# Kernel optimization log

Measured on AMD Instinct MI355X. Metric: run time of the kernel, lower is better.

## Reference

```python
import jax, jax.numpy as jnp
import numpy as np

N = 20000      # nodes per graph
E = 320000     # edges per graph (before self-loops)
G = 256        # graphs (strings) per side
VOCAB = 128    # NUMBER_EMBEDDINGS
D_IN = 128
HID = 64
H = 4
D_OUT = 128
NEG_SLOPE = 0.2  # PyG GATConv leaky_relu slope


def _gat(x, edge_index, W, att_s, att_d, bias, concat):
    """PyG GATConv: gather -> per-edge logits -> segment softmax over dst -> scatter.
    x: [N, F_in], W: [F_in, H*C], att_s/att_d: [H, C], bias: [H*C] or [C].
    Self-loops are added (PyG default add_self_loops=True)."""
    n = x.shape[0]
    h, c = att_s.shape
    loops = jnp.arange(n)
    src = jnp.concatenate([edge_index[0], loops])  # message sources j
    dst = jnp.concatenate([edge_index[1], loops])  # message targets i
    xh = (x @ W).reshape(n, h, c)                  # [N,H,C]
    a_s = jnp.einsum('nhc,hc->nh', xh, att_s)      # [N,H]
    a_d = jnp.einsum('nhc,hc->nh', xh, att_d)
    logits = jax.nn.leaky_relu(a_s[src] + a_d[dst], NEG_SLOPE)  # [E',H]
    m = jax.ops.segment_max(logits, dst, num_segments=n)
    m = jnp.where(jnp.isfinite(m), m, 0.0)
    e = jnp.exp(logits - m[dst])
    z = jax.ops.segment_sum(e, dst, num_segments=n)
    alpha = e / (z[dst] + 1e-16)                   # [E',H]
    msg = xh[src] * alpha[:, :, None]              # [E',H,C]
    out = jax.ops.segment_sum(msg, dst, num_segments=n)  # [N,H,C]
    out = out.reshape(n, h * c) if concat else out.mean(axis=1)
    return out + bias


def _encode(xi, ei, batch, emb, W1, as1, ad1, b1, lw1, lb1,
            W2, as2, ad2, b2, lw2, lb2, W3, as3, ad3, b3, lw3, lb3):
    e = emb[xi]  # [N, D_IN]
    x = jax.nn.relu(_gat(e, ei, W1, as1, ad1, b1, True) + e @ lw1 + lb1)
    x = jax.nn.relu(_gat(x, ei, W2, as2, ad2, b2, True) + x @ lw2 + lb2)
    x = _gat(x, ei, W3, as3, ad3, b3, False) + x @ lw3 + lb3  # [N, D_OUT]
    s = jax.ops.segment_sum(x, batch, num_segments=G)
    cnt = jax.ops.segment_sum(jnp.ones((x.shape[0],), x.dtype), batch, num_segments=G)
    return s / jnp.maximum(cnt, 1.0)[:, None]  # global_mean_pool -> [G, D_OUT]


def setup_inputs() -> dict:
    key = jax.random.key(0)
    ks = jax.random.split(key, 32)
    hc = H * HID  # 256
    def nrm(k, shape, scale=0.05):
        return jax.random.normal(k, shape, dtype=jnp.float32) * scale
    inp = {
        'x_l': jax.random.randint(ks[0], (N,), 0, VOCAB),
        'edge_l': jax.random.randint(ks[1], (2, E), 0, N),
        'batch_l': jnp.sort(jax.random.randint(ks[2], (N,), 0, G)),
        'x_r': jax.random.randint(ks[3], (N,), 0, VOCAB),
        'edge_r': jax.random.randint(ks[4], (2, E), 0, N),
        'batch_r': jnp.sort(jax.random.randint(ks[5], (N,), 0, G)),
        'emb': nrm(ks[6], (VOCAB, D_IN), 1.0),
        'W1': nrm(ks[7], (D_IN, hc)), 'as1': nrm(ks[8], (H, HID)), 'ad1': nrm(ks[9], (H, HID)),
        'b1': jnp.zeros((hc,), jnp.float32), 'lw1': nrm(ks[10], (D_IN, hc)), 'lb1': jnp.zeros((hc,), jnp.float32),
        'W2': nrm(ks[11], (hc, hc)), 'as2': nrm(ks[12], (H, HID)), 'ad2': nrm(ks[13], (H, HID)),
        'b2': jnp.zeros((hc,), jnp.float32), 'lw2': nrm(ks[14], (hc, hc)), 'lb2': jnp.zeros((hc,), jnp.float32),
        'W3': nrm(ks[15], (hc, H * D_OUT)), 'as3': nrm(ks[16], (H, D_OUT)), 'ad3': nrm(ks[17], (H, D_OUT)),
        'b3': jnp.zeros((D_OUT,), jnp.float32), 'lw3': nrm(ks[18], (hc, D_OUT)), 'lb3': jnp.zeros((D_OUT,), jnp.float32),
    }
    return inp


def reference(x_l, edge_l, batch_l, x_r, edge_r, batch_r, emb,
              W1, as1, ad1, b1, lw1, lb1,
              W2, as2, ad2, b2, lw2, lb2,
              W3, as3, ad3, b3, lw3, lb3):
    params = (emb, W1, as1, ad1, b1, lw1, lb1, W2, as2, ad2, b2, lw2, lb2,
              W3, as3, ad3, b3, lw3, lb3)
    out_l = _encode(x_l, edge_l, batch_l, *params)
    out_r = _encode(x_r, edge_r, batch_r, *params)
    return (out_l, out_r)
```

## Files before the change

kernel.cpp:

```cpp
#include <hip/hip_runtime.h>

#define GG 256

typedef __bf16 bf16x8 __attribute__((ext_vector_type(8)));
typedef float floatx4 __attribute__((ext_vector_type(4)));
typedef float f32x2 __attribute__((ext_vector_type(2)));

__device__ __forceinline__ float lrelu(float x) { return x > 0.f ? x : 0.2f * x; }

__device__ __forceinline__ void wt1(const float* __restrict__ B, __bf16* __restrict__ Bt,
                                    int K, int M, int idx) {
    int k = idx / M, m = idx - k * M;
    Bt[(size_t)m * K + k] = (__bf16)B[idx];
}
__device__ __forceinline__ void wattn1(const float* __restrict__ W,
                                       const float* __restrict__ as_,
                                       const float* __restrict__ ad_,
                                       __bf16* __restrict__ dst, int K, int C, int idx) {
    int j = idx / K, k = idx - j * K;
    float v = 0.f;
    if (j < 8) {
        int h = j & 3;
        const float* att = (j < 4) ? as_ : ad_;
        int M = 4 * C;
        for (int c = 0; c < C; c++) v += W[(size_t)k * M + h * C + c] * att[h * C + c];
    }
    dst[(size_t)j * K + k] = (__bf16)v;
}

__global__ void k_wprep(const float* W1, const float* lw1, const float* as1, const float* ad1,
                        const float* W2, const float* lw2, const float* as2, const float* ad2,
                        const float* W3, const float* lw3, const float* as3, const float* ad3,
                        __bf16* B1t, __bf16* B2t, __bf16* B3t) {
    int idx = blockIdx.x * blockDim.x + threadIdx.x;
    if (idx < 32768) { wt1(W1, B1t, 128, 256, idx); return; }
    idx -= 32768;
    if (idx < 32768) { wt1(lw1, B1t + 256 * 128, 128, 256, idx); return; }
    idx -= 32768;
    if (idx < 2048) { wattn1(W1, as1, ad1, B1t + 512 * 128, 128, 64, idx); return; }
    idx -= 2048;
    if (idx < 65536) { wt1(W2, B2t, 256, 256, idx); return; }
    idx -= 65536;
    if (idx < 65536) { wt1(lw2, B2t + 256 * 256, 256, 256, idx); return; }
    idx -= 65536;
    if (idx < 4096) { wattn1(W2, as2, ad2, B2t + 512 * 256, 256, 64, idx); return; }
    idx -= 4096;
    if (idx < 131072) { wt1(W3, B3t, 256, 512, idx); return; }
    idx -= 131072;
    if (idx < 32768) { wt1(lw3, B3t + 512 * 256, 256, 128, idx); return; }
    idx -= 32768;
    if (idx < 4096) { wattn1(W3, as3, ad3, B3t + 640 * 256, 256, 128, idx); return; }
}

template <int K, bool EMB>
__global__ __launch_bounds__(256) void k_gemm_all(const __bf16* __restrict__ A,
                                                  const int* __restrict__ xl,
                                                  const int* __restrict__ xr,
                                                  const float* __restrict__ emb,
                                                  const __bf16* __restrict__ Bt,
                                                  int n, int n1, int Mx, int Ml,
                                                  unsigned char* __restrict__ x8, int ldx,
                                                  float* __restrict__ lin, int ldl,
                                                  const float* __restrict__ bias1,
                                                  const float* __restrict__ bias2,
                                                  float* __restrict__ a_s,
                                                  float* __restrict__ a_d) {
    constexpr int KS = K / 32;
    constexpr int LDK = K + 8;
    constexpr int LPR = K / 8;
    constexpr int NCH = 64 * LPR / 256;
    __shared__ __bf16 S[64 * LDK];
    int tid = threadIdx.x;
    int wave = tid >> 6, lane = tid & 63;
    int row0 = blockIdx.x * 64;
#pragma unroll
    for (int c = 0; c < NCH; c++) {
        int i = tid + c * 256;
        int r = i / LPR, ko = (i - r * LPR) * 8;
        int gr = row0 + r;
        bf16x8 v = {};
        if (gr < n) {
            if (EMB) {
                int xi = (gr < n1) ? xl[gr] : xr[gr - n1];
                const float4* src = (const float4*)(emb + ((size_t)xi << 7) + ko);
                float4 q0 = src[0], q1 = src[1];
                v = bf16x8{(__bf16)q0.x, (__bf16)q0.y, (__bf16)q0.z, (__bf16)q0.w,
                           (__bf16)q1.x, (__bf16)q1.y, (__bf16)q1.z, (__bf16)q1.w};
            } else {
                v = *(const bf16x8*)(A + (size_t)gr * K + ko);
            }
        }
        *(bf16x8*)&S[r * LDK + ko] = v;
    }
    __syncthreads();
    int kOff = (lane >> 4) * 8;
    int colBase = lane & 15;
    bf16x8 af[KS];
#pragma unroll
    for (int ks = 0; ks < KS; ks++)
        af[ks] = *(const bf16x8*)&S[(wave * 16 + colBase) * LDK + ks * 32 + kOff];
    int Mtot = Mx + Ml;
    int gr0 = row0 + wave * 16 + ((lane >> 4) << 2);
    int half = (Mtot / 128) * 64;
    int c0beg = blockIdx.y * half;
    int T = half / 64;
    bf16x8 regs[NCH];
#pragma unroll
    for (int c = 0; c < NCH; c++) {
        int i = tid + c * 256;
        int r = i / LPR, ko = (i - r * LPR) * 8;
        regs[c] = *(const bf16x8*)(Bt + (size_t)(c0beg + r) * K + ko);
    }
    for (int t = 0; t < T; t++) {
        __syncthreads();
#pragma unroll
        for (int c = 0; c < NCH; c++) {
            int i = tid + c * 256;
            int r = i / LPR, ko = (i - r * LPR) * 8;
            *(bf16x8*)&S[r * LDK + ko] = regs[c];
        }
        if (t + 1 < T) {
            int c0n = c0beg + (t + 1) * 64;
#pragma unroll
            for (int c = 0; c < NCH; c++) {
                int i = tid + c * 256;
                int r = i / LPR, ko = (i - r * LPR) * 8;
                regs[c] = *(const bf16x8*)(Bt + (size_t)(c0n + r) * K + ko);
            }
        }
        __syncthreads();
        floatx4 acc[4] = {};
#pragma unroll
        for (int ct = 0; ct < 4; ct++) {
#pragma unroll
            for (int ks = 0; ks < KS; ks++) {
                bf16x8 bf = *(const bf16x8*)&S[(ct * 16 + colBase) * LDK + ks * 32 + kOff];
                acc[ct] = __builtin_amdgcn_mfma_f32_16x16x32_bf16(af[ks], bf, acc[ct], 0, 0, 0);
            }
        }
        int c0 = c0beg + t * 64;
        if (c0 < Mx) {
#pragma unroll
            for (int r = 0; r < 4; r++) {
                int gr = gr0 + r;
                if (gr >= n) continue;
#pragma unroll
                for (int ct = 0; ct < 4; ct++) {
                    float v = acc[ct][r];
                    int p = __builtin_amdgcn_cvt_pk_fp8_f32(v, v, 0, false);
                    x8[(size_t)gr * ldx + c0 + ct * 16 + colBase] = (unsigned char)(p & 0xff);
                }
            }
        } else {
#pragma unroll
            for (int r = 0; r < 4; r++) {
                int gr = gr0 + r;
                if (gr >= n) continue;
#pragma unroll
                for (int ct = 0; ct < 4; ct++) {
                    int c2 = c0 + ct * 16 + colBase - Mx;
                    float v = acc[ct][r] + bias1[c2];
                    if (bias2) v += bias2[c2];
                    lin[(size_t)gr * ldl + c2] = v;
                }
            }
        }
    }
    if (blockIdx.y == 1) {
        floatx4 acc = {};
        const __bf16* bp = Bt + (size_t)(Mtot + colBase) * K + kOff;
#pragma unroll
        for (int ks = 0; ks < KS; ks++) {
            bf16x8 bf = *(const bf16x8*)(bp + ks * 32);
            acc = __builtin_amdgcn_mfma_f32_16x16x32_bf16(af[ks], bf, acc, 0, 0, 0);
        }
        if (colBase < 8) {
            float* dst = (colBase < 4) ? a_s : a_d;
            int h = colBase & 3;
#pragma unroll
            for (int r = 0; r < 4; r++) {
                int gr = gr0 + r;
                if (gr < n) dst[gr * 4 + h] = acc[r];
            }
        }
    }
}

__global__ void k_hist2(const int* __restrict__ el, const int* __restrict__ er,
                        int E, int n, int* __restrict__ deg) {
    int e = blockIdx.x * blockDim.x + threadIdx.x;
    if (e >= 2 * E) return;
    int d = (e < E) ? el[E + e] : er[E + (e - E)] + n;
    atomicAdd(&deg[d], 1);
}

__global__ __launch_bounds__(1024) void k_scan(int* __restrict__ rp, int n) {
    __shared__ int wsum[16];
    __shared__ int s_carry;
    int lane = threadIdx.x & 63, wid = threadIdx.x >> 6;
    if (threadIdx.x == 0) s_carry = 0;
    __syncthreads();
    for (int base = 0; base < n; base += 1024) {
        int i = base + threadIdx.x;
        int v = (i < n) ? rp[i] : 0;
        int inc = v;
#pragma unroll
        for (int off = 1; off < 64; off <<= 1) {
            int t = __shfl_up(inc, off, 64);
            if (lane >= off) inc += t;
        }
        if (lane == 63) wsum[wid] = inc;
        __syncthreads();
        int carry = s_carry;
        __syncthreads();
        if (wid == 0) {
            int wv = (lane < 16) ? wsum[lane] : 0;
            int winc = wv;
#pragma unroll
            for (int off = 1; off < 16; off <<= 1) {
                int t = __shfl_up(winc, off, 64);
                if (lane >= off) winc += t;
            }
            if (lane < 16) wsum[lane] = winc - wv;
            if (lane == 15) s_carry = carry + winc;
        }
        __syncthreads();
        if (i < n) rp[i] = carry + wsum[wid] + (inc - v);
        __syncthreads();
    }
}

__global__ void k_fill2(const int* __restrict__ el, const int* __restrict__ er,
                        int E, int n, int* __restrict__ rp, int* __restrict__ csr) {
    int e = blockIdx.x * blockDim.x + threadIdx.x;
    if (e >= 2 * E) return;
    int d, s;
    if (e < E) { s = el[e]; d = el[E + e]; }
    else       { s = er[e - E] + n; d = er[E + (e - E)] + n; }
    int pos = atomicAdd(&rp[d], 1);
    csr[pos] = s;
}

__device__ __forceinline__ void dec4(unsigned int u, float* f) {
    f32x2 a = __builtin_amdgcn_cvt_pk_f32_fp8(u, false);
    f32x2 b = __builtin_amdgcn_cvt_pk_f32_fp8(u, true);
    f[0] = a[0]; f[1] = a[1]; f[2] = b[0]; f[3] = b[1];
}

__global__ __launch_bounds__(256) void k_agg12(const int* __restrict__ rp,
                                               const int* __restrict__ csr,
                                               const float* __restrict__ a_s,
                                               const float* __restrict__ a_d,
                                               const unsigned char* __restrict__ x8,
                                               const float* __restrict__ lin,
                                               __bf16* __restrict__ out_bf, int n) {
    int wv = (int)((blockIdx.x * blockDim.x + threadIdx.x) >> 6);
    int lane = threadIdx.x & 63;
    int sub = lane >> 5, sl = lane & 31;
    int node = wv * 2 + sub;
    if (node >= n) return;
    int c0 = sl * 8;
    int h = sl >> 3;
    int start = node ? rp[node - 1] : 0;
    int end = rp[node];
    float ad = a_d[node * 4 + h];
    float z = __expf(lrelu(a_s[node * 4 + h] + ad));
    float acc[8];
    {
        uint2 u = *(const uint2*)(x8 + (size_t)node * 256 + c0);
        float f[8];
        dec4(u.x, f); dec4(u.y, f + 4);
#pragma unroll
        for (int j = 0; j < 8; j++) acc[j] = z * f[j];
    }
    uint2 u0 = {}, u1 = {};
    float A0 = 0.f, A1 = 0.f;
    if (start < end) {
        int s = csr[start];
        u0 = *(const uint2*)(x8 + (size_t)s * 256 + c0);
        A0 = a_s[s * 4 + h];
    }
    if (start + 1 < end) {
        int s = csr[start + 1];
        u1 = *(const uint2*)(x8 + (size_t)s * 256 + c0);
        A1 = a_s[s * 4 + h];
    }
    for (int e = start; e < end; e++) {
        uint2 uc = u0;
        float ac = A0;
        u0 = u1; A0 = A1;
        if (e + 2 < end) {
            int s = csr[e + 2];
            u1 = *(const uint2*)(x8 + (size_t)s * 256 + c0);
            A1 = a_s[s * 4 + h];
        }
        float w = __expf(lrelu(ac + ad));
        z += w;
        float f[8];
        dec4(uc.x, f); dec4(uc.y, f + 4);
#pragma unroll
        for (int q = 0; q < 8; q++) acc[q] += w * f[q];
    }
    float inv = 1.f / (z + 1e-16f);
    const float4* lp = (const float4*)(lin + (size_t)node * 256 + c0);
    float4 l0 = lp[0], l1 = lp[1];
    float lf[8] = {l0.x, l0.y, l0.z, l0.w, l1.x, l1.y, l1.z, l1.w};
    bf16x8 r;
#pragma unroll
    for (int j = 0; j < 8; j++)
        r[j] = (__bf16)fmaxf(acc[j] * inv + lf[j], 0.f);
    *(bf16x8*)(out_bf + (size_t)node * 256 + c0) = r;
}

__global__ __launch_bounds__(256) void k_agg3(const int* __restrict__ rp,
                                              const int* __restrict__ csr,
                                              const float* __restrict__ a_s,
                                              const float* __restrict__ a_d,
                                              const unsigned int* __restrict__ x8,
                                              float* __restrict__ mean, int n) {
    int wv = (int)((blockIdx.x * blockDim.x + threadIdx.x) >> 6);
    int lane = threadIdx.x & 63;
    int sub = lane >> 5, sl = lane & 31;
    int node = wv * 2 + sub;
    if (node >= n) return;
    int h = sl >> 3;
    int start = node ? rp[node - 1] : 0;
    int end = rp[node];
    float ad = a_d[node * 4 + h];
    float z = __expf(lrelu(a_s[node * 4 + h] + ad));
    float acc[16];
    {
        uint4 u = *(const uint4*)(x8 + (size_t)node * 128 + sl * 4);
        float f[16];
        dec4(u.x, f); dec4(u.y, f + 4); dec4(u.z, f + 8); dec4(u.w, f + 12);
#pragma unroll
        for (int j = 0; j < 16; j++) acc[j] = z * f[j];
    }
    uint4 u0 = {}, u1 = {};
    float A0 = 0.f, A1 = 0.f;
    if (start < end) {
        int s = csr[start];
        u0 = *(const uint4*)(x8 + (size_t)s * 128 + sl * 4);
        A0 = a_s[s * 4 + h];
    }
    if (start + 1 < end) {
        int s = csr[start + 1];
        u1 = *(const uint4*)(x8 + (size_t)s * 128 + sl * 4);
        A1 = a_s[s * 4 + h];
    }
    for (int e = start; e < end; e++) {
        uint4 uc = u0;
        float ac = A0;
        u0 = u1; A0 = A1;
        if (e + 2 < end) {
            int s = csr[e + 2];
            u1 = *(const uint4*)(x8 + (size_t)s * 128 + sl * 4);
            A1 = a_s[s * 4 + h];
        }
        float w = __expf(lrelu(ac + ad));
        z += w;
        float f[16];
        dec4(uc.x, f); dec4(uc.y, f + 4); dec4(uc.z, f + 8); dec4(uc.w, f + 12);
#pragma unroll
        for (int q = 0; q < 16; q++) acc[q] += w * f[q];
    }
    float scale = 0.25f / (z + 1e-16f);
#pragma unroll
    for (int j = 0; j < 16; j++) {
        float v = acc[j] * scale;
        v += __shfl_xor(v, 8, 64);
        v += __shfl_xor(v, 16, 64);
        acc[j] = v;
    }
    if ((sl & 24) == 0) {
        float4* op = (float4*)(mean + (size_t)node * 128 + sl * 16);
#pragma unroll
        for (int q = 0; q < 4; q++) {
            float4 o = {acc[4 * q], acc[4 * q + 1], acc[4 * q + 2], acc[4 * q + 3]};
            op[q] = o;
        }
    }
}

__global__ __launch_bounds__(128) void k_pool(const float* __restrict__ mean,
                                              const float* __restrict__ lin3,
                                              const float* __restrict__ b3,
                                              const int* __restrict__ bl,
                                              const int* __restrict__ br,
                                              int n, float* __restrict__ out) {
    int g = blockIdx.x, c = threadIdx.x;
    const int* b = (g < GG) ? bl : br;
    int tg = (g < GG) ? g : g - GG;
    int off = (g < GG) ? 0 : n;
    int s, e;
    { int lo = 0, hi = n; while (lo < hi) { int m = (lo + hi) >> 1; if (b[m] < tg) lo = m + 1; else hi = m; } s = lo; }
    { int lo = 0, hi = n; while (lo < hi) { int m = (lo + hi) >> 1; if (b[m] < tg + 1) lo = m + 1; else hi = m; } e = lo; }
    s += off; e += off;
    float acc = 0.f;
    for (int i = s; i < e; i++)
        acc += mean[(size_t)i * 128 + c] + lin3[(size_t)i * 128 + c];
    int cnt = e - s;
    out[(size_t)g * 128 + c] = cnt > 0 ? acc / (float)cnt + b3[c] : 0.f;
}

static inline int cdiv(int a, int b) { return (a + b - 1) / b; }

extern "C" void kernel_launch(void* const* d_in, const int* in_sizes, int n_in,
                              void* d_out, int out_size, void* d_ws, size_t ws_size,
                              hipStream_t stream) {
    const int* x_l = (const int*)d_in[0];
    const int* edge_l = (const int*)d_in[1];
    const int* batch_l = (const int*)d_in[2];
    const int* x_r = (const int*)d_in[3];
    const int* edge_r = (const int*)d_in[4];
    const int* batch_r = (const int*)d_in[5];
    const float* emb = (const float*)d_in[6];
    const float* W1 = (const float*)d_in[7];
    const float* as1 = (const float*)d_in[8];
    const float* ad1 = (const float*)d_in[9];
    const float* b1 = (const float*)d_in[10];
    const float* lw1 = (const float*)d_in[11];
    const float* lb1 = (const float*)d_in[12];
    const float* W2 = (const float*)d_in[13];
    const float* as2 = (const float*)d_in[14];
    const float* ad2 = (const float*)d_in[15];
    const float* b2 = (const float*)d_in[16];
    const float* lw2 = (const float*)d_in[17];
    const float* lb2 = (const float*)d_in[18];
    const float* W3 = (const float*)d_in[19];
    const float* as3 = (const float*)d_in[20];
    const float* ad3 = (const float*)d_in[21];
    const float* b3 = (const float*)d_in[22];
    const float* lw3 = (const float*)d_in[23];
    const float* lb3 = (const float*)d_in[24];

    const int n = in_sizes[0];
    const int E = in_sizes[1] / 2;
    const int N2 = 2 * n;

    float* MEAN = (float*)d_ws;
    float* LIN = MEAN + (size_t)N2 * 128;
    float* L3 = LIN + (size_t)N2 * 256;
    float* a_s = L3 + (size_t)N2 * 128;
    float* a_d = a_s + (size_t)N2 * 4;
    int* rp = (int*)(a_d + (size_t)N2 * 4);
    int* csr = rp + N2;
    unsigned char* X8a = (unsigned char*)(csr + 2 * E);
    unsigned char* X8b = X8a + (size_t)N2 * 256;
    __bf16* Abf = (__bf16*)(X8b + (size_t)N2 * 512);
    __bf16* B1t = Abf + (size_t)N2 * 256;
    __bf16* B2t = B1t + 528 * 128;
    __bf16* B3t = B2t + 528 * 256;

    const int TB = 256;
    dim3 blk(TB);

    k_wprep<<<cdiv(370688, TB), blk, 0, stream>>>(W1, lw1, as1, ad1, W2, lw2, as2, ad2,
                                                  W3, lw3, as3, ad3, B1t, B2t, B3t);

    hipMemsetAsync(rp, 0, sizeof(int) * (size_t)N2, stream);
    k_hist2<<<cdiv(2 * E, TB), blk, 0, stream>>>(edge_l, edge_r, E, n, rp);
    k_scan<<<1, 1024, 0, stream>>>(rp, N2);
    k_fill2<<<cdiv(2 * E, TB), blk, 0, stream>>>(edge_l, edge_r, E, n, rp, csr);

    k_gemm_all<128, true><<<dim3(cdiv(N2, 64), 2), blk, 0, stream>>>(
        nullptr, x_l, x_r, emb, B1t, N2, n, 256, 256, X8a, 256, LIN, 256, lb1, b1, a_s, a_d);
    k_agg12<<<cdiv(N2, 8), blk, 0, stream>>>(rp, csr, a_s, a_d, X8a, LIN, Abf, N2);

    k_gemm_all<256, false><<<dim3(cdiv(N2, 64), 2), blk, 0, stream>>>(
        Abf, nullptr, nullptr, nullptr, B2t, N2, n, 256, 256, X8a, 256, LIN, 256, lb2, b2, a_s, a_d);
    k_agg12<<<cdiv(N2, 8), blk, 0, stream>>>(rp, csr, a_s, a_d, X8a, LIN, Abf, N2);

    k_gemm_all<256, false><<<dim3(cdiv(N2, 64), 2), blk, 0, stream>>>(
        Abf, nullptr, nullptr, nullptr, B3t, N2, n, 512, 128, X8b, 512, L3, 128, lb3, nullptr, a_s, a_d);
    k_agg3<<<cdiv(N2, 8), blk, 0, stream>>>(rp, csr, a_s, a_d, (const unsigned int*)X8b, MEAN, N2);
    k_pool<<<2 * GG, 128, 0, stream>>>(MEAN, L3, b3, batch_l, batch_r, n, (float*)d_out);
}
```

Before: 498.8 us.

## Enlarge GEMM row tile, store linear branch in bf16, one node per wave

Each GEMM block now covers 128 rows instead of 64, with two MFMA row tiles per wave sharing each B fragment, which halves B-tile reloads per output. The layer 1 and 2 linear/residual outputs are stored as bf16 rather than fp32, cutting write and read traffic. The aggregation kernels now give each node a full 64-lane wave instead of half a wave, with a deeper 3-edge prefetch pipeline. The trade-offs are more registers and LDS per GEMM block, fewer GEMM blocks, and some precision loss in the residual path.

```diff
diff --git a/kernel.cpp b/kernel.cpp
--- a/kernel.cpp
+++ b/kernel.cpp
@@ -3,6 +3,7 @@
 #define GG 256
 
 typedef __bf16 bf16x8 __attribute__((ext_vector_type(8)));
+typedef __bf16 bf16x4 __attribute__((ext_vector_type(4)));
 typedef float floatx4 __attribute__((ext_vector_type(4)));
 typedef float f32x2 __attribute__((ext_vector_type(2)));
 
@@ -52,7 +53,7 @@
     if (idx < 4096) { wattn1(W3, as3, ad3, B3t + 640 * 256, 256, 128, idx); return; }
 }
 
-template <int K, bool EMB>
+template <int K, bool EMB, bool LINBF>
 __global__ __launch_bounds__(256) void k_gemm_all(const __bf16* __restrict__ A,
                                                   const int* __restrict__ xl,
                                                   const int* __restrict__ xr,
@@ -60,7 +61,8 @@
                                                   const __bf16* __restrict__ Bt,
                                                   int n, int n1, int Mx, int Ml,
                                                   unsigned char* __restrict__ x8, int ldx,
-                                                  float* __restrict__ lin, int ldl,
+                                                  float* __restrict__ linf,
+                                                  __bf16* __restrict__ linb, int ldl,
                                                   const float* __restrict__ bias1,
                                                   const float* __restrict__ bias2,
                                                   float* __restrict__ a_s,
@@ -68,13 +70,14 @@
     constexpr int KS = K / 32;
     constexpr int LDK = K + 8;
     constexpr int LPR = K / 8;
-    constexpr int NCH = 64 * LPR / 256;
-    __shared__ __bf16 S[64 * LDK];
+    constexpr int NCHA = 128 * LPR / 256;
+    constexpr int NCHB = 64 * LPR / 256;
+    __shared__ __bf16 S[128 * LDK];
     int tid = threadIdx.x;
     int wave = tid >> 6, lane = tid & 63;
-    int row0 = blockIdx.x * 64;
-#pragma unroll
-    for (int c = 0; c < NCH; c++) {
+    int row0 = blockIdx.x * 128;
+#pragma unroll
+    for (int c = 0; c < NCHA; c++) {
         int i = tid + c * 256;
         int r = i / LPR, ko = (i - r * LPR) * 8;
         int gr = row0 + r;
@@ -95,18 +98,20 @@
     __syncthreads();
     int kOff = (lane >> 4) * 8;
     int colBase = lane & 15;
-    bf16x8 af[KS];
-#pragma unroll
-    for (int ks = 0; ks < KS; ks++)
-        af[ks] = *(const bf16x8*)&S[(wave * 16 + colBase) * LDK + ks * 32 + kOff];
+    bf16x8 af[2][KS];
+#pragma unroll
+    for (int rt = 0; rt < 2; rt++)
+#pragma unroll
+        for (int ks = 0; ks < KS; ks++)
+            af[rt][ks] = *(const bf16x8*)&S[(wave * 32 + rt * 16 + colBase) * LDK + ks * 32 + kOff];
     int Mtot = Mx + Ml;
-    int gr0 = row0 + wave * 16 + ((lane >> 4) << 2);
+    int gr0 = row0 + wave * 32 + ((lane >> 4) << 2);
     int half = (Mtot / 128) * 64;
     int c0beg = blockIdx.y * half;
     int T = half / 64;
-    bf16x8 regs[NCH];
-#pragma unroll
-    for (int c = 0; c < NCH; c++) {
+    bf16x8 regs[NCHB];
+#pragma unroll
+    for (int c = 0; c < NCHB; c++) {
         int i = tid + c * 256;
         int r = i / LPR, ko = (i - r * LPR) * 8;
         regs[c] = *(const bf16x8*)(Bt + (size_t)(c0beg + r) * K + ko);
@@ -114,7 +119,7 @@
     for (int t = 0; t < T; t++) {
         __syncthreads();
 #pragma unroll
-        for (int c = 0; c < NCH; c++) {
+        for (int c = 0; c < NCHB; c++) {
             int i = tid + c * 256;
             int r = i / LPR, ko = (i - r * LPR) * 8;
             *(bf16x8*)&S[r * LDK + ko] = regs[c];
@@ -122,66 +127,77 @@
         if (t + 1 < T) {
             int c0n = c0beg + (t + 1) * 64;
 #pragma unroll
-            for (int c = 0; c < NCH; c++) {
+            for (int c = 0; c < NCHB; c++) {
                 int i = tid + c * 256;
                 int r = i / LPR, ko = (i - r * LPR) * 8;
                 regs[c] = *(const bf16x8*)(Bt + (size_t)(c0n + r) * K + ko);
             }
         }
         __syncthreads();
-        floatx4 acc[4] = {};
+        floatx4 acc[2][4] = {};
 #pragma unroll
         for (int ct = 0; ct < 4; ct++) {
 #pragma unroll
             for (int ks = 0; ks < KS; ks++) {
                 bf16x8 bf = *(const bf16x8*)&S[(ct * 16 + colBase) * LDK + ks * 32 + kOff];
-                acc[ct] = __builtin_amdgcn_mfma_f32_16x16x32_bf16(af[ks], bf, acc[ct], 0, 0, 0);
+#pragma unroll
+                for (int rt = 0; rt < 2; rt++)
+                    acc[rt][ct] = __builtin_amdgcn_mfma_f32_16x16x32_bf16(af[rt][ks], bf, acc[rt][ct], 0, 0, 0);
             }
         }
         int c0 = c0beg + t * 64;
         if (c0 < Mx) {
 #pragma unroll
-            for (int r = 0; r < 4; r++) {
-                int gr = gr0 + r;
-                if (gr >= n) continue;
-#pragma unroll
-                for (int ct = 0; ct < 4; ct++) {
-                    float v = acc[ct][r];
-                    int p = __builtin_amdgcn_cvt_pk_fp8_f32(v, v, 0, false);
-                    x8[(size_t)gr * ldx + c0 + ct * 16 + colBase] = (unsigned char)(p & 0xff);
+            for (int rt = 0; rt < 2; rt++)
+#pragma unroll
+                for (int r = 0; r < 4; r++) {
+                    int gr = gr0 + rt * 16 + r;
+                    if (gr >= n) continue;
+#pragma unroll
+                    for (int ct = 0; ct < 4; ct++) {
+                        float v = acc[rt][ct][r];
+                        int p = __builtin_amdgcn_cvt_pk_fp8_f32(v, v, 0, false);
+                        x8[(size_t)gr * ldx + c0 + ct * 16 + colBase] = (unsigned char)(p & 0xff);
+                    }
                 }
-            }
         } else {
 #pragma unroll
-            for (int r = 0; r < 4; r++) {
-                int gr = gr0 + r;
-                if (gr >= n) continue;
-#pragma unroll
-                for (int ct = 0; ct < 4; ct++) {
-                    int c2 = c0 + ct * 16 + colBase - Mx;
-                    float v = acc[ct][r] + bias1[c2];
-                    if (bias2) v += bias2[c2];
-                    lin[(size_t)gr * ldl + c2] = v;
+            for (int rt = 0; rt < 2; rt++)
+#pragma unroll
+                for (int r = 0; r < 4; r++) {
+                    int gr = gr0 + rt * 16 + r;
+                    if (gr >= n) continue;
+#pragma unroll
+                    for (int ct = 0; ct < 4; ct++) {
+                        int c2 = c0 + ct * 16 + colBase - Mx;
+                        float v = acc[rt][ct][r] + bias1[c2];
+                        if (bias2) v += bias2[c2];
+                        if (LINBF) linb[(size_t)gr * ldl + c2] = (__bf16)v;
+                        else       linf[(size_t)gr * ldl + c2] = v;
+                    }
                 }
-            }
         }
     }
     if (blockIdx.y == 1) {
-        floatx4 acc = {};
+        floatx4 acc2[2] = {};
         const __bf16* bp = Bt + (size_t)(Mtot + colBase) * K + kOff;
 #pragma unroll
         for (int ks = 0; ks < KS; ks++) {
             bf16x8 bf = *(const bf16x8*)(bp + ks * 32);
-            acc = __builtin_amdgcn_mfma_f32_16x16x32_bf16(af[ks], bf, acc, 0, 0, 0);
+#pragma unroll
+            for (int rt = 0; rt < 2; rt++)
+                acc2[rt] = __builtin_amdgcn_mfma_f32_16x16x32_bf16(af[rt][ks], bf, acc2[rt], 0, 0, 0);
         }
         if (colBase < 8) {
             float* dst = (colBase < 4) ? a_s : a_d;
             int h = colBase & 3;
 #pragma unroll
-            for (int r = 0; r < 4; r++) {
-                int gr = gr0 + r;
-                if (gr < n) dst[gr * 4 + h] = acc[r];
-            }
+            for (int rt = 0; rt < 2; rt++)
+#pragma unroll
+                for (int r = 0; r < 4; r++) {
+                    int gr = gr0 + rt * 16 + r;
+                    if (gr < n) dst[gr * 4 + h] = acc2[rt][r];
+                }
         }
     }
 }
@@ -252,47 +268,117 @@
                                                const float* __restrict__ a_s,
                                                const float* __restrict__ a_d,
                                                const unsigned char* __restrict__ x8,
-                                               const float* __restrict__ lin,
+                                               const __bf16* __restrict__ lin,
                                                __bf16* __restrict__ out_bf, int n) {
-    int wv = (int)((blockIdx.x * blockDim.x + threadIdx.x) >> 6);
+    int node = (int)((blockIdx.x * blockDim.x + threadIdx.x) >> 6);
+    if (node >= n) return;
     int lane = threadIdx.x & 63;
-    int sub = lane >> 5, sl = lane & 31;
-    int node = wv * 2 + sub;
+    int c0 = lane * 4;
+    int h = lane >> 4;
+    int start = node ? rp[node - 1] : 0;
+    int end = rp[node];
+    float ad = a_d[node * 4 + h];
+    float z = __expf(lrelu(a_s[node * 4 + h] + ad));
+    float acc[4];
+    {
+        unsigned int u = *(const unsigned int*)(x8 + (size_t)node * 256 + c0);
+        float f[4];
+        dec4(u, f);
+#pragma unroll
+        for (int j = 0; j < 4; j++) acc[j] = z * f[j];
+    }
+    unsigned int u0 = 0, u1 = 0, u2 = 0;
+    float A0 = 0.f, A1 = 0.f, A2 = 0.f;
+    if (start < end) {
+        int s = csr[start];
+        u0 = *(const unsigned int*)(x8 + (size_t)s * 256 + c0);
+        A0 = a_s[s * 4 + h];
+    }
+    if (start + 1 < end) {
+        int s = csr[start + 1];
+        u1 = *(const unsigned int*)(x8 + (size_t)s * 256 + c0);
+        A1 = a_s[s * 4 + h];
+    }
+    if (start + 2 < end) {
+        int s = csr[start + 2];
+        u2 = *(const unsigned int*)(x8 + (size_t)s * 256 + c0);
+        A2 = a_s[s * 4 + h];
+    }
+    for (int e = start; e < end; e++) {
+        unsigned int uc = u0;
+        float ac = A0;
+        u0 = u1; A0 = A1;
+        u1 = u2; A1 = A2;
+        if (e + 3 < end) {
+            int s = csr[e + 3];
+            u2 = *(const unsigned int*)(x8 + (size_t)s * 256 + c0);
+            A2 = a_s[s * 4 + h];
+        }
+        float w = __expf(lrelu(ac + ad));
+        z += w;
+        float f[4];
+        dec4(uc, f);
+#pragma unroll
+        for (int q = 0; q < 4; q++) acc[q] += w * f[q];
+    }
+    float inv = 1.f / (z + 1e-16f);
+    bf16x4 l = *(const bf16x4*)(lin + (size_t)node * 256 + c0);
+    bf16x4 r;
+#pragma unroll
+    for (int j = 0; j < 4; j++)
+        r[j] = (__bf16)fmaxf(acc[j] * inv + (float)l[j], 0.f);
+    *(bf16x4*)(out_bf + (size_t)node * 256 + c0) = r;
+}
+
+__global__ __launch_bounds__(256) void k_agg3(const int* __restrict__ rp,
+                                              const int* __restrict__ csr,
+                                              const float* __restrict__ a_s,
+                                              const float* __restrict__ a_d,
+                                              const unsigned char* __restrict__ x8,
+                                              float* __restrict__ mean, int n) {
+    int node = (int)((blockIdx.x * blockDim.x + threadIdx.x) >> 6);
     if (node >= n) return;
-    int c0 = sl * 8;
-    int h = sl >> 3;
+    int lane = threadIdx.x & 63;
+    int c0 = lane * 8;
+    int h = lane >> 4;
     int start = node ? rp[node - 1] : 0;
     int end = rp[node];
     float ad = a_d[node * 4 + h];
     float z = __expf(lrelu(a_s[node * 4 + h] + ad));
     float acc[8];
     {
-        uint2 u = *(const uint2*)(x8 + (size_t)node * 256 + c0);
+        uint2 u = *(const uint2*)(x8 + (size_t)node * 512 + c0);
         float f[8];
         dec4(u.x, f); dec4(u.y, f + 4);
 #pragma unroll
         for (int j = 0; j < 8; j++) acc[j] = z * f[j];
     }
-    uint2 u0 = {}, u1 = {};
-    float A0 = 0.f, A1 = 0.f;
+    uint2 u0 = {}, u1 = {}, u2 = {};
+    float A0 = 0.f, A1 = 0.f, A2 = 0.f;
     if (start < end) {
         int s = csr[start];
-        u0 = *(const uint2*)(x8 + (size_t)s * 256 + c0);
+        u0 = *(const uint2*)(x8 + (size_t)s * 512 + c0);
         A0 = a_s[s * 4 + h];
     }
     if (start + 1 < end) {
         int s = csr[start + 1];
-        u1 = *(const uint2*)(x8 + (size_t)s * 256 + c0);
+        u1 = *(const uint2*)(x8 + (size_t)s * 512 + c0);
         A1 = a_s[s * 4 + h];
+    }
+    if (start + 2 < end) {
+        int s = csr[start + 2];
+        u2 = *(const uint2*)(x8 + (size_t)s * 512 + c0);
+        A2 = a_s[s * 4 + h];
     }
     for (int e = start; e < end; e++) {
         uint2 uc = u0;
         float ac = A0;
         u0 = u1; A0 = A1;
-        if (e + 2 < end) {
-            int s = csr[e + 2];
-            u1 = *(const uint2*)(x8 + (size_t)s * 256 + c0);
-            A1 = a_s[s * 4 + h];
+        u1 = u2; A1 = A2;
+        if (e + 3 < end) {
+            int s = csr[e + 3];
+            u2 = *(const uint2*)(x8 + (size_t)s * 512 + c0);
+            A2 = a_s[s * 4 + h];
         }
         float w = __expf(lrelu(ac + ad));
         z += w;
@@ -301,84 +387,19 @@
 #pragma unroll
         for (int q = 0; q < 8; q++) acc[q] += w * f[q];
     }
-    float inv = 1.f / (z + 1e-16f);
-    const float4* lp = (const float4*)(lin + (size_t)node * 256 + c0);
-    float4 l0 = lp[0], l1 = lp[1];
-    float lf[8] = {l0.x, l0.y, l0.z, l0.w, l1.x, l1.y, l1.z, l1.w};
-    bf16x8 r;
-#pragma unroll
-    for (int j = 0; j < 8; j++)
-        r[j] = (__bf16)fmaxf(acc[j] * inv + lf[j], 0.f);
-    *(bf16x8*)(out_bf + (size_t)node * 256 + c0) = r;
-}
-
-__global__ __launch_bounds__(256) void k_agg3(const int* __restrict__ rp,
-                                              const int* __restrict__ csr,
-                                              const float* __restrict__ a_s,
-                                              const float* __restrict__ a_d,
-                                              const unsigned int* __restrict__ x8,
-                                              float* __restrict__ mean, int n) {
-    int wv = (int)((blockIdx.x * blockDim.x + threadIdx.x) >> 6);
-    int lane = threadIdx.x & 63;
-    int sub = lane >> 5, sl = lane & 31;
-    int node = wv * 2 + sub;
-    if (node >= n) return;
-    int h = sl >> 3;
-    int start = node ? rp[node - 1] : 0;
-    int end = rp[node];
-    float ad = a_d[node * 4 + h];
-    float z = __expf(lrelu(a_s[node * 4 + h] + ad));
-    float acc[16];
-    {
-        uint4 u = *(const uint4*)(x8 + (size_t)node * 128 + sl * 4);
-        float f[16];
-        dec4(u.x, f); dec4(u.y, f + 4); dec4(u.z, f + 8); dec4(u.w, f + 12);
-#pragma unroll
-        for (int j = 0; j < 16; j++) acc[j] = z * f[j];
-    }
-    uint4 u0 = {}, u1 = {};
-    float A0 = 0.f, A1 = 0.f;
-    if (start < end) {
-        int s = csr[start];
-        u0 = *(const uint4*)(x8 + (size_t)s * 128 + sl * 4);
-        A0 = a_s[s * 4 + h];
-    }
-    if (start + 1 < end) {
-        int s = csr[start + 1];
-        u1 = *(const uint4*)(x8 + (size_t)s * 128 + sl * 4);
-        A1 = a_s[s * 4 + h];
-    }
-    for (int e = start; e < end; e++) {
-        uint4 uc = u0;
-        float ac = A0;
-        u0 = u1; A0 = A1;
-        if (e + 2 < end) {
-            int s = csr[e + 2];
-            u1 = *(const uint4*)(x8 + (size_t)s * 128 + sl * 4);
-            A1 = a_s[s * 4 + h];
-        }
-        float w = __expf(lrelu(ac + ad));
-        z += w;
-        float f[16];
-        dec4(uc.x, f); dec4(uc.y, f + 4); dec4(uc.z, f + 8); dec4(uc.w, f + 12);
-#pragma unroll
-        for (int q = 0; q < 16; q++) acc[q] += w * f[q];
-    }
     float scale = 0.25f / (z + 1e-16f);
 #pragma unroll
-    for (int j = 0; j < 16; j++) {
+    for (int j = 0; j < 8; j++) {
         float v = acc[j] * scale;
-        v += __shfl_xor(v, 8, 64);
         v += __shfl_xor(v, 16, 64);
+        v += __shfl_xor(v, 32, 64);
         acc[j] = v;
     }
-    if ((sl & 24) == 0) {
-        float4* op = (float4*)(mean + (size_t)node * 128 + sl * 16);
-#pragma unroll
-        for (int q = 0; q < 4; q++) {
-            float4 o = {acc[4 * q], acc[4 * q + 1], acc[4 * q + 2], acc[4 * q + 3]};
-            op[q] = o;
-        }
+    if (lane < 16) {
+        float4* op = (float4*)(mean + (size_t)node * 128 + lane * 8);
+        float4 o0 = {acc[0], acc[1], acc[2], acc[3]};
+        float4 o1 = {acc[4], acc[5], acc[6], acc[7]};
+        op[0] = o0; op[1] = o1;
     }
 }
 
@@ -439,13 +460,13 @@
     const int N2 = 2 * n;
 
     float* MEAN = (float*)d_ws;
-    float* LIN = MEAN + (size_t)N2 * 128;
-    float* L3 = LIN + (size_t)N2 * 256;
+    float* L3 = MEAN + (size_t)N2 * 128;
     float* a_s = L3 + (size_t)N2 * 128;
     float* a_d = a_s + (size_t)N2 * 4;
     int* rp = (int*)(a_d + (size_t)N2 * 4);
     int* csr = rp + N2;
-    unsigned char* X8a = (unsigned char*)(csr + 2 * E);
+    __bf16* LINb = (__bf16*)(csr + 2 * E);
+    unsigned char* X8a = (unsigned char*)(LINb + (size_t)N2 * 256);
     unsigned char* X8b = X8a + (size_t)N2 * 256;
     __bf16* Abf = (__bf16*)(X8b + (size_t)N2 * 512);
     __bf16* B1t = Abf + (size_t)N2 * 256;
@@ -463,16 +484,16 @@
     k_scan<<<1, 1024, 0, stream>>>(rp, N2);
     k_fill2<<<cdiv(2 * E, TB), blk, 0, stream>>>(edge_l, edge_r, E, n, rp, csr);
 
-    k_gemm_all<128, true><<<dim3(cdiv(N2, 64), 2), blk, 0, stream>>>(
-        nullptr, x_l, x_r, emb, B1t, N2, n, 256, 256, X8a, 256, LIN, 256, lb1, b1, a_s, a_d);
-    k_agg12<<<cdiv(N2, 8), blk, 0, stream>>>(rp, csr, a_s, a_d, X8a, LIN, Abf, N2);
-
-    k_gemm_all<256, false><<<dim3(cdiv(N2, 64), 2), blk, 0, stream>>>(
-        Abf, nullptr, nullptr, nullptr, B2t, N2, n, 256, 256, X8a, 256, LIN, 256, lb2, b2, a_s, a_d);
-    k_agg12<<<cdiv(N2, 8), blk, 0, stream>>>(rp, csr, a_s, a_d, X8a, LIN, Abf, N2);
-
-    k_gemm_all<256, false><<<dim3(cdiv(N2, 64), 2), blk, 0, stream>>>(
-        Abf, nullptr, nullptr, nullptr, B3t, N2, n, 512, 128, X8b, 512, L3, 128, lb3, nullptr, a_s, a_d);
-    k_agg3<<<cdiv(N2, 8), blk, 0, stream>>>(rp, csr, a_s, a_d, (const unsigned int*)X8b, MEAN, N2);
+    k_gemm_all<128, true, true><<<dim3(cdiv(N2, 128), 2), blk, 0, stream>>>(
+        nullptr, x_l, x_r, emb, B1t, N2, n, 256, 256, X8a, 256, nullptr, LINb, 256, lb1, b1, a_s, a_d);
+    k_agg12<<<cdiv(N2 * 64, TB), blk, 0, stream>>>(rp, csr, a_s, a_d, X8a, LINb, Abf, N2);
+
+    k_gemm_all<256, false, true><<<dim3(cdiv(N2, 128), 2), blk, 0, stream>>>(
+        Abf, nullptr, nullptr, nullptr, B2t, N2, n, 256, 256, X8a, 256, nullptr, LINb, 256, lb2, b2, a_s, a_d);
+    k_agg12<<<cdiv(N2 * 64, TB), blk, 0, stream>>>(rp, csr, a_s, a_d, X8a, LINb, Abf, N2);
+
+    k_gemm_all<256, false, false><<<dim3(cdiv(N2, 128), 2), blk, 0, stream>>>(
+        Abf, nullptr, nullptr, nullptr, B3t, N2, n, 512, 128, X8b, 512, L3, nullptr, 128, lb3, nullptr, a_s, a_d);
+    k_agg3<<<cdiv(N2 * 64, TB), blk, 0, stream>>>(rp, csr, a_s, a_d, X8b, MEAN, N2);
     k_pool<<<2 * GG, 128, 0, stream>>>(MEAN, L3, b3, batch_l, batch_r, n, (float*)d_out);
 }
```

Result: slower. 588.8 us (+18.0%).
